# Performance work log

Hardware: AMD Instinct MI355X
Metric: run time of the kernel (lower is better)

## Reference

```python
import jax, jax.numpy as jnp
import numpy as np

NF = 64   # num_feat
DG = 8    # deformable_groups (also conv groups)
B, H, W = 4, 96, 96
K = 9     # 3x3 kernel positions


def _conv(x, w, b, padding=1, dilation=1, groups=1):
    out = jax.lax.conv_general_dilated(
        x, w, (1, 1), [(padding, padding), (padding, padding)],
        rhs_dilation=(dilation, dilation),
        dimension_numbers=('NCHW', 'OIHW', 'NCHW'),
        feature_group_count=groups)
    return out + b[None, :, None, None]


def _lrelu(t):
    return jnp.where(t >= 0, t, 0.1 * t)


def _cat_align(a, b):
    # channel-interleaved concat: [a0,b0,a1,b1,...]
    Bn, k, h, w = a.shape
    return jnp.stack([a, b], axis=2).reshape(Bn, 2 * k, h, w)


def _deform_conv(x, offset, mask, weight, bias, dilation, padding):
    # DCNv2 modulated deformable conv, stride 1.
    Bn, C, h, w = x.shape
    Cpg = C // DG
    off = offset.reshape(Bn, DG, K, 2, h, w)          # (dy, dx) per group/kernel pos
    m = mask.reshape(Bn, DG, K, h, w)
    ky = (jnp.repeat(jnp.arange(3), 3) * dilation - padding).astype(x.dtype)  # (K,)
    kx = (jnp.tile(jnp.arange(3), 3) * dilation - padding).astype(x.dtype)
    hs = jnp.arange(h, dtype=x.dtype)
    ws = jnp.arange(w, dtype=x.dtype)
    py = off[:, :, :, 0] + ky[None, None, :, None, None] + hs[None, None, None, :, None]
    px = off[:, :, :, 1] + kx[None, None, :, None, None] + ws[None, None, None, None, :]
    y0f = jnp.floor(py); x0f = jnp.floor(px)
    ly = (py - y0f)[:, :, None]  # broadcast over Cpg
    lx = (px - x0f)[:, :, None]
    y0 = y0f.astype(jnp.int32); x0 = x0f.astype(jnp.int32)
    xg = x.reshape(Bn, DG, Cpg, h * w)

    def gather(yi, xi):
        inb = ((yi >= 0) & (yi < h) & (xi >= 0) & (xi < w))
        idx = (jnp.clip(yi, 0, h - 1) * w + jnp.clip(xi, 0, w - 1)).reshape(Bn, DG, 1, K * h * w)
        v = jnp.take_along_axis(xg, jnp.broadcast_to(idx, (Bn, DG, Cpg, K * h * w)), axis=3)
        return v.reshape(Bn, DG, Cpg, K, h, w) * inb[:, :, None].astype(x.dtype)

    v00 = gather(y0, x0); v01 = gather(y0, x0 + 1)
    v10 = gather(y0 + 1, x0); v11 = gather(y0 + 1, x0 + 1)
    val = (v00 * (1 - ly) * (1 - lx) + v01 * (1 - ly) * lx
           + v10 * ly * (1 - lx) + v11 * ly * lx) * m[:, :, None]
    sampled = val.reshape(Bn, C, K, h, w)
    out = jnp.einsum('bckhw,ock->bohw', sampled, weight.reshape(weight.shape[0], C, K))
    return out + bias[None, :, None, None]


def _dcn(x, off_feat, om_w, om_b, w, b, dilation):
    pad = dilation  # int(3/2)*dilation
    out = _conv(off_feat, om_w, om_b, padding=pad, dilation=dilation)
    o1, o2, msk = jnp.split(out, 3, axis=1)
    offset = jnp.concatenate([o1, o2], axis=1)
    mask = jax.nn.sigmoid(msk)
    return _deform_conv(x, offset, mask, w, b, dilation, pad)


def setup_inputs() -> dict:
    key = jax.random.key(0)
    ks = iter(jax.random.split(key, 64))
    def rn(shape, s=0.05):
        return jax.random.normal(next(ks), shape, jnp.float32) * s
    d = {}
    d['nbr_feat'] = jax.random.normal(next(ks), (B, NF, H, W), jnp.float32)
    d['ref_feat'] = jax.random.normal(next(ks), (B, NF, H, W), jnp.float32)
    for lv, has3 in [('l3', False), ('l2', True), ('l1', True)]:
        d[f'oc1_w_{lv}'] = rn((NF, 2 * NF // DG, 3, 3)); d[f'oc1_b_{lv}'] = rn((NF,))
        oc2_in = 2 * NF if has3 else NF
        d[f'oc2_w_{lv}'] = rn((NF, oc2_in // DG, 3, 3)); d[f'oc2_b_{lv}'] = rn((NF,))
        if has3:
            d[f'oc3_w_{lv}'] = rn((NF, NF // DG, 3, 3)); d[f'oc3_b_{lv}'] = rn((NF,))
            d[f'fc_w_{lv}'] = rn((NF, 2 * NF // DG, 3, 3)); d[f'fc_b_{lv}'] = rn((NF,))
        d[f'om_w_{lv}'] = rn((DG * 3 * K, NF, 3, 3), 0.01); d[f'om_b_{lv}'] = rn((DG * 3 * K,), 0.01)
        d[f'dcn_w_{lv}'] = rn((NF, NF, 3, 3)); d[f'dcn_b_{lv}'] = rn((NF,))
    d['cas_oc1_w'] = rn((NF, 2 * NF // DG, 3, 3)); d['cas_oc1_b'] = rn((NF,))
    d['cas_oc2_w'] = rn((NF, NF // DG, 3, 3)); d['cas_oc2_b'] = rn((NF,))
    d['cas_om_w'] = rn((DG * 3 * K, NF, 3, 3), 0.01); d['cas_om_b'] = rn((DG * 3 * K,), 0.01)
    d['cas_w'] = rn((NF, NF, 3, 3)); d['cas_b'] = rn((NF,))
    return d


def reference(nbr_feat, ref_feat,
              oc1_w_l3, oc1_b_l3, oc2_w_l3, oc2_b_l3, om_w_l3, om_b_l3, dcn_w_l3, dcn_b_l3,
              oc1_w_l2, oc1_b_l2, oc2_w_l2, oc2_b_l2, oc3_w_l2, oc3_b_l2, fc_w_l2, fc_b_l2,
              om_w_l2, om_b_l2, dcn_w_l2, dcn_b_l2,
              oc1_w_l1, oc1_b_l1, oc2_w_l1, oc2_b_l1, oc3_w_l1, oc3_b_l1, fc_w_l1, fc_b_l1,
              om_w_l1, om_b_l1, dcn_w_l1, dcn_b_l1,
              cas_oc1_w, cas_oc1_b, cas_oc2_w, cas_oc2_b, cas_om_w, cas_om_b, cas_w, cas_b):
    # level 3 (dilation 5)
    off = _lrelu(_conv(_cat_align(nbr_feat, ref_feat), oc1_w_l3, oc1_b_l3, groups=DG))
    off = _lrelu(_conv(off, oc2_w_l3, oc2_b_l3, groups=DG))
    feat = _lrelu(_dcn(nbr_feat, off, om_w_l3, om_b_l3, dcn_w_l3, dcn_b_l3, 5))
    to, tf = off, feat
    # level 2 (dilation 3)
    off = _lrelu(_conv(_cat_align(nbr_feat, ref_feat), oc1_w_l2, oc1_b_l2, groups=DG))
    off = _lrelu(_conv(_cat_align(off, to), oc2_w_l2, oc2_b_l2, groups=DG))
    off = _lrelu(_conv(off, oc3_w_l2, oc3_b_l2, groups=DG))
    feat = _dcn(nbr_feat, off, om_w_l2, om_b_l2, dcn_w_l2, dcn_b_l2, 3)
    feat = _lrelu(_conv(_cat_align(feat, tf), fc_w_l2, fc_b_l2, groups=DG))
    to, tf = off, feat
    # level 1 (dilation 1), no lrelu on feat
    off = _lrelu(_conv(_cat_align(nbr_feat, ref_feat), oc1_w_l1, oc1_b_l1, groups=DG))
    off = _lrelu(_conv(_cat_align(off, to), oc2_w_l1, oc2_b_l1, groups=DG))
    off = _lrelu(_conv(off, oc3_w_l1, oc3_b_l1, groups=DG))
    feat = _dcn(nbr_feat, off, om_w_l1, om_b_l1, dcn_w_l1, dcn_b_l1, 1)
    feat = _conv(_cat_align(feat, tf), fc_w_l1, fc_b_l1, groups=DG)
    # cascade
    off = _cat_align(feat, ref_feat)
    off = _lrelu(_conv(_lrelu(_conv(off, cas_oc1_w, cas_oc1_b, groups=DG)), cas_oc2_w, cas_oc2_b, groups=DG))
    feat = _lrelu(_dcn(feat, off, cas_om_w, cas_om_b, cas_w, cas_b, 1))
    return feat
```

## Files before the change

### kernel.cpp

```cpp
#include <hip/hip_runtime.h>

#define BATCH 4
#define NFEAT 64
#define DGRP 8
#define HH 96
#define WW 96
#define HWP (HH*WW)

typedef short short4a __attribute__((ext_vector_type(4)));
typedef short short8 __attribute__((ext_vector_type(8)));
typedef float f32x4 __attribute__((ext_vector_type(4)));
typedef float f32x16 __attribute__((ext_vector_type(16)));

__device__ inline short f2bf(float f) {
  union { float f; unsigned u; } v; v.f = f;
  unsigned r = v.u + 0x7fff + ((v.u >> 16) & 1);
  return (short)(r >> 16);
}
__device__ inline float bf2f(short s) {
  return __uint_as_float(((unsigned)(unsigned short)s) << 16);
}

__global__ __launch_bounds__(256) void prep_om(
    const float* __restrict__ s0, const float* __restrict__ s1,
    const float* __restrict__ s2, const float* __restrict__ s3,
    short* __restrict__ dst) {
  int gid = blockIdx.x * 256 + threadIdx.x;
  if (gid >= 4 * 147456) return;
  int t = gid / 147456, r = gid % 147456;
  int tile = r / 18432, r2 = r % 18432;
  int kk = r2 / 512, r3 = r2 % 512;
  int lane = r3 / 8, j = r3 % 8;
  int col = lane & 31, half = lane >> 5;
  int oc = tile * 32 + col;
  int k = kk * 16 + half * 8 + j;
  int p = k >> 6, c = k & 63;
  const float* s = (t == 0) ? s0 : (t == 1) ? s1 : (t == 2) ? s2 : s3;
  float v = (oc < 216) ? s[(size_t)oc * 576 + c * 9 + p] : 0.f;
  dst[gid] = f2bf(v);
}

__global__ __launch_bounds__(256) void prep_dcnw(
    const float* __restrict__ s0, const float* __restrict__ s1,
    const float* __restrict__ s2, const float* __restrict__ s3,
    short* __restrict__ dst) {
  int gid = blockIdx.x * 256 + threadIdx.x;
  if (gid >= 4 * 36864) return;
  int t = gid / 36864, r = gid % 36864;
  int tile = r / 18432, r2 = r % 18432;
  int kk = r2 / 512, r3 = r2 % 512;
  int lane = r3 / 8, j = r3 % 8;
  int col = lane & 31, half = lane >> 5;
  int oc = tile * 32 + col;
  int k = kk * 16 + half * 8 + j;
  int p = k >> 6, c = k & 63;
  const float* s = (t == 0) ? s0 : (t == 1) ? s1 : (t == 2) ? s2 : s3;
  dst[gid] = f2bf(s[(size_t)oc * 576 + c * 9 + p]);
}

struct GwArgs {
  const float* src[12];
  int cat[12];
  int base[13];
};

__global__ __launch_bounds__(256) void prep_gw(GwArgs a, short* __restrict__ dst) {
  int gid = blockIdx.x * 256 + threadIdx.x;
  if (gid >= a.base[12]) return;
  int t = 0;
  while (gid >= a.base[t + 1]) ++t;
  int r = gid - a.base[t];
  const float* s = a.src[t];
  const int tsz = a.cat[t] ? 4608 : 2560;
  int tile = r / tsz, r2 = r % tsz;
  int kk = r2 / 512, r3 = r2 % 512;
  int lane = r3 >> 3, j = r3 & 7;
  int m = lane & 15, quad = lane >> 4;
  int oc = tile * 16 + m;
  int j32 = quad * 8 + j;
  float val = 0.f;
  if (a.cat[t]) {
    int gsel = j32 >> 4, ssel = (j32 >> 3) & 1, ch8 = j32 & 7;
    if (gsel == (m >> 3)) val = s[oc * 144 + (2 * ch8 + ssel) * 9 + kk];
  } else {
    int tapsel = j32 >> 4, gsel = (j32 >> 3) & 1, ch8 = j32 & 7;
    int p = 2 * kk + tapsel;
    if (p < 9 && gsel == (m >> 3)) val = s[oc * 72 + ch8 * 9 + p];
  }
  dst[gid] = f2bf(val);
}

__global__ __launch_bounds__(256) void transpose_bf16(
    const float* __restrict__ in0, short* __restrict__ out0,
    const float* __restrict__ in1, short* __restrict__ out1) {
  const float* in = blockIdx.z ? in1 : in0;
  short* out = blockIdx.z ? out1 : out0;
  __shared__ float s[64][65];
  const int p0 = blockIdx.x * 64;
  const int b = blockIdx.y;
  const int tx = threadIdx.x, ty = threadIdx.y;
  for (int c = ty; c < 64; c += 4)
    s[c][tx] = in[((size_t)b * NFEAT + c) * HWP + p0 + tx];
  __syncthreads();
  for (int p = ty; p < 64; p += 4)
    out[((size_t)b * HWP + p0 + p) * NFEAT + tx] = f2bf(s[tx][p]);
}

template <bool CAT, bool LRELU>
__device__ __forceinline__ void gconv_body(
    const short* __restrict__ in0, const short* __restrict__ in1,
    const short* __restrict__ Wsh, const float* __restrict__ bias,
    short* __restrict__ out, int pixbase, int b) {
  const int lane = threadIdx.x, t = threadIdx.y;
  const int n = lane & 15, quad = lane >> 4;
  constexpr int NKK = CAT ? 9 : 5;

  short8 A[NKK];
#pragma unroll
  for (int kk = 0; kk < NKK; ++kk)
    A[kk] = *(const short8*)(Wsh + ((size_t)(t * NKK + kk) * 64 + lane) * 8);

  const short* sb;
  if (CAT) {
    sb = ((quad & 1) ? in1 : in0) + (size_t)b * HWP * 64 + (2 * t + (quad >> 1)) * 8;
  } else {
    sb = in0 + (size_t)b * HWP * 64 + (2 * t + (quad & 1)) * 8;
  }

  f32x4 acc[2] = {};
#pragma unroll
  for (int nt = 0; nt < 2; ++nt) {
    const int pix = pixbase + nt * 16 + n;
    const int yp = pix / WW, xp = pix % WW;
#pragma unroll
    for (int kk = 0; kk < NKK; ++kk) {
      const int p = CAT ? kk : (2 * kk + (quad >> 1));
      short8 B = {0, 0, 0, 0, 0, 0, 0, 0};
      if (p < 9) {
        const int sy = yp + p / 3 - 1, sx = xp + p % 3 - 1;
        if (((unsigned)sy < (unsigned)HH) && ((unsigned)sx < (unsigned)WW))
          B = *(const short8*)(sb + (size_t)(sy * WW + sx) * 64);
      }
      acc[nt] = __builtin_amdgcn_mfma_f32_16x16x32_bf16(A[kk], B, acc[nt], 0, 0, 0);
    }
  }

  const int ocb = t * 16 + quad * 4;
  const float b0 = bias[ocb], b1 = bias[ocb + 1], b2 = bias[ocb + 2], b3 = bias[ocb + 3];
#pragma unroll
  for (int nt = 0; nt < 2; ++nt) {
    float v0 = acc[nt][0] + b0, v1 = acc[nt][1] + b1;
    float v2 = acc[nt][2] + b2, v3 = acc[nt][3] + b3;
    if (LRELU) {
      v0 = (v0 >= 0.f) ? v0 : 0.1f * v0;
      v1 = (v1 >= 0.f) ? v1 : 0.1f * v1;
      v2 = (v2 >= 0.f) ? v2 : 0.1f * v2;
      v3 = (v3 >= 0.f) ? v3 : 0.1f * v3;
    }
    short4a pk = {f2bf(v0), f2bf(v1), f2bf(v2), f2bf(v3)};
    *(short4a*)(out + ((size_t)b * HWP + pixbase + nt * 16 + n) * 64 + ocb) = pk;
  }
}

template <bool CAT, bool LRELU>
__global__ __launch_bounds__(256) void gconv_mfma(
    const short* __restrict__ in0, const short* __restrict__ in1,
    const short* __restrict__ Wsh, const float* __restrict__ bias,
    short* __restrict__ out) {
  gconv_body<CAT, LRELU>(in0, in1, Wsh, bias, out, blockIdx.x * 32, blockIdx.y);
}

struct Oc1Args {
  const short* W[3];
  const float* bias[3];
  short* out[3];
};

__global__ __launch_bounds__(256) void gconv_oc1x3(
    const short* __restrict__ in0, const short* __restrict__ in1, Oc1Args a) {
  const int job = blockIdx.z;
  gconv_body<true, true>(in0, in1, a.W[job], a.bias[job], a.out[job],
                         blockIdx.x * 32, blockIdx.y);
}

template <int D, bool LRELU, bool PMOUT>
__global__ __launch_bounds__(256) void omdcn_fused(
    const short* __restrict__ omIn,
    const short* __restrict__ xT,
    const short* __restrict__ Wom,
    const float* __restrict__ obias,
    const short* __restrict__ Wd,
    const float* __restrict__ bias,
    void* __restrict__ outv) {
  __shared__ __align__(16) char smem[18432 + 13824];
  short* Ls = (short*)smem;
  short* om_lds = (short*)(smem + 18432);
  float* red = (float*)(smem + 18432);

  const int tx = threadIdx.x, ty = threadIdx.y;
  const int lid = ty * 32 + tx;
  const int lane = lid & 63, w = lid >> 6;
  const int col = lane & 31, half = lane >> 5;
  const int pb = blockIdx.x, b = blockIdx.y;
  const int pixbase = pb * 32;

  {
    const short* pixb = omIn + (size_t)b * HWP * 64;
    const short* aP0 = Wom + ((size_t)(w * 36) * 64 + lane) * 8;
    const short* aP1 = Wom + ((size_t)((w + 4) * 36) * 64 + lane) * 8;
    const int pix = pixbase + col;
    const int yp = pix / WW, xp = pix % WW;
    f32x16 acc0 = {}, acc1 = {};
#pragma unroll
    for (int p = 0; p < 9; ++p) {
      const int sy = yp + (p / 3 - 1) * D, sx = xp + (p % 3 - 1) * D;
      const bool valid = ((unsigned)sy < (unsigned)HH) && ((unsigned)sx < (unsigned)WW);
      const short* bsrc = pixb + (size_t)(sy * WW + sx) * 64 + half * 8;
#pragma unroll
      for (int q = 0; q < 4; ++q) {
        const int kk = p * 4 + q;
        short8 B = {0, 0, 0, 0, 0, 0, 0, 0};
        if (valid) B = *(const short8*)(bsrc + q * 16);
        short8 A0 = *(const short8*)(aP0 + (size_t)kk * 512);
        short8 A1 = *(const short8*)(aP1 + (size_t)kk * 512);
        acc0 = __builtin_amdgcn_mfma_f32_32x32x16_bf16(A0, B, acc0, 0, 0, 0);
        acc1 = __builtin_amdgcn_mfma_f32_32x32x16_bf16(A1, B, acc1, 0, 0, 0);
      }
    }
#pragma unroll
    for (int r = 0; r < 16; ++r) {
      const int rrow = (r & 3) + 8 * (r >> 2) + 4 * half;
      const int oc0 = w * 32 + rrow;
      om_lds[oc0 * 32 + col] = f2bf(acc0[r] + obias[oc0]);
      const int oc1 = (w + 4) * 32 + rrow;
      if (oc1 < 216)
        om_lds[oc1 * 32 + col] = f2bf(acc1[r] + obias[oc1]);
    }
  }
  __syncthreads();

  const int dg = ty;
  const int pixS = pixbase + tx;
  const int ypS = pixS / WW, xpS = pixS % WW;
  const short* xb = xT + (size_t)b * HWP * 64 + dg * 8;
  short* Sp = Ls + (size_t)((dg & 1) * 32 + tx) * 8;

  auto sample_k = [&](int k, int slotbase) {
    float dy = bf2f(om_lds[(dg * 18 + 2 * k) * 32 + tx]);
    float dxv = bf2f(om_lds[(dg * 18 + 2 * k + 1) * 32 + tx]);
    float mr = bf2f(om_lds[(144 + dg * 9 + k) * 32 + tx]);
    float m = 1.f / (1.f + __expf(-mr));
    float py = (float)(ypS + (k / 3 - 1) * D) + dy;
    float px_ = (float)(xpS + (k % 3 - 1) * D) + dxv;
    float y0f = floorf(py), x0f = floorf(px_);
    float ly = py - y0f, lx = px_ - x0f;
    int y0 = (int)y0f, x0 = (int)x0f;
    int y1 = y0 + 1, x1 = x0 + 1;
    bool vy0 = (unsigned)y0 < (unsigned)HH, vy1 = (unsigned)y1 < (unsigned)HH;
    bool vx0 = (unsigned)x0 < (unsigned)WW, vx1 = (unsigned)x1 < (unsigned)WW;
    int cy0 = min(max(y0, 0), HH - 1), cy1 = min(max(y1, 0), HH - 1);
    int cx0 = min(max(x0, 0), WW - 1), cx1 = min(max(x1, 0), WW - 1);
    float w00 = (vy0 && vx0) ? (1.f - ly) * (1.f - lx) * m : 0.f;
    float w01 = (vy0 && vx1) ? (1.f - ly) * lx * m : 0.f;
    float w10 = (vy1 && vx0) ? ly * (1.f - lx) * m : 0.f;
    float w11 = (vy1 && vx1) ? ly * lx * m : 0.f;
    short8 s00 = *(const short8*)(xb + (size_t)(cy0 * WW + cx0) * 64);
    short8 s01 = *(const short8*)(xb + (size_t)(cy0 * WW + cx1) * 64);
    short8 s10 = *(const short8*)(xb + (size_t)(cy1 * WW + cx0) * 64);
    short8 s11 = *(const short8*)(xb + (size_t)(cy1 * WW + cx1) * 64);
    short8 pk;
#pragma unroll
    for (int cl = 0; cl < 8; ++cl) {
      float v = w00 * bf2f(s00[cl]) + w01 * bf2f(s01[cl]) +
                w10 * bf2f(s10[cl]) + w11 * bf2f(s11[cl]);
      pk[cl] = f2bf(v);
    }
    const int slot = k * 4 + (dg >> 1) - slotbase;
    *(short8*)(Sp + (size_t)slot * 512) = pk;
  };

  const int octile = w & 1, kh = w >> 1;
  const short* aPd = Wd + ((size_t)(octile * 36) * 64 + lane) * 8;
  const short* bPd = Ls + (size_t)lane * 8;
  f32x16 accd = {};

#pragma unroll
  for (int k = 0; k < 4; ++k) sample_k(k, 0);
  if (dg < 4) sample_k(4, 0);
  __syncthreads();
#pragma unroll
  for (int i = 0; i < 9; ++i) {
    const int kkg = kh * 9 + i;
    short8 A = *(const short8*)(aPd + (size_t)kkg * 512);
    short8 B = *(const short8*)(bPd + (size_t)kkg * 512);
    accd = __builtin_amdgcn_mfma_f32_32x32x16_bf16(A, B, accd, 0, 0, 0);
  }
  __syncthreads();

  if (dg >= 4) sample_k(4, 18);
#pragma unroll
  for (int k = 5; k < 9; ++k) sample_k(k, 18);
  __syncthreads();
#pragma unroll
  for (int i = 0; i < 9; ++i) {
    const int kkg = 18 + kh * 9 + i;
    const int kkl = kh * 9 + i;
    short8 A = *(const short8*)(aPd + (size_t)kkg * 512);
    short8 B = *(const short8*)(bPd + (size_t)kkl * 512);
    accd = __builtin_amdgcn_mfma_f32_32x32x16_bf16(A, B, accd, 0, 0, 0);
  }

  const int pix = pixbase + col;
  if (kh == 1) {
#pragma unroll
    for (int r = 0; r < 16; ++r) red[(octile * 64 + lane) * 17 + r] = accd[r];
  }
  __syncthreads();
  if (kh == 0) {
    if (PMOUT) {
      short* out = (short*)outv;
#pragma unroll
      for (int rg = 0; rg < 4; ++rg) {
        short4a pk;
#pragma unroll
        for (int i = 0; i < 4; ++i) {
          const int r = rg * 4 + i;
          const int oc = octile * 32 + i + 8 * rg + 4 * half;
          float v = accd[r] + red[(octile * 64 + lane) * 17 + r] + bias[oc];
          if (LRELU) v = (v >= 0.f) ? v : 0.1f * v;
          pk[i] = f2bf(v);
        }
        *(short4a*)(out + ((size_t)b * HWP + pix) * 64 + octile * 32 + 8 * rg + 4 * half) = pk;
      }
    } else {
      float* out = (float*)outv;
#pragma unroll
      for (int r = 0; r < 16; ++r) {
        const int oc = octile * 32 + (r & 3) + 8 * (r >> 2) + 4 * half;
        float v = accd[r] + red[(octile * 64 + lane) * 17 + r] + bias[oc];
        if (LRELU) v = (v >= 0.f) ? v : 0.1f * v;
        out[((size_t)b * NFEAT + oc) * HWP + pix] = v;
      }
    }
  }
}

extern "C" void kernel_launch(void* const* d_in, const int* in_sizes, int n_in,
                              void* d_out, int out_size, void* d_ws, size_t ws_size,
                              hipStream_t stream) {
  const float* nbr = (const float*)d_in[0];
  const float* ref = (const float*)d_in[1];
  auto f = [&](int i) { return (const float*)d_in[i]; };

  short* s0 = (short*)d_ws;
  const size_t PM = (size_t)BATCH * HWP * 64;
  short* omB = s0;
  short* refT = omB + 7962624;
  short* pmA = refT + PM;
  short* pmB = pmA + PM;
  short* pmC = pmB + PM;
  short* pmD = pmC + PM;
  short* pmE = pmD + PM;
  short* pmF = pmE + PM;
  short* pmG = pmF + PM;
  short* wbf = pmG + PM;
  short* wdcn = wbf + 589824;
  short* wgc = wdcn + 147456;
  short* nbrT = (short*)d_out;

  prep_om<<<(4 * 147456 + 255) / 256, 256, 0, stream>>>(f(6), f(18), f(30), f(38), wbf);
  prep_dcnw<<<(4 * 36864 + 255) / 256, 256, 0, stream>>>(f(8), f(20), f(32), f(40), wdcn);

  static const int gSrc[12] = {2, 4, 10, 12, 14, 16, 22, 24, 26, 28, 34, 36};
  static const int gCat[12] = {1, 0, 1, 1, 0, 1, 1, 1, 0, 1, 1, 0};
  GwArgs ga;
  int gb = 0;
  const short* wg[12];
  for (int t = 0; t < 12; ++t) {
    ga.src[t] = f(gSrc[t]);
    ga.cat[t] = gCat[t];
    ga.base[t] = gb;
    wg[t] = wgc + gb;
    gb += gCat[t] ? 18432 : 10240;
  }
  ga.base[12] = gb;
  prep_gw<<<(gb + 255) / 256, 256, 0, stream>>>(ga, wgc);

  short* wbf_l3 = wbf;
  short* wbf_l2 = wbf + 147456;
  short* wbf_l1 = wbf + 2 * 147456;
  short* wbf_cas = wbf + 3 * 147456;
  short* wd_l3 = wdcn;
  short* wd_l2 = wdcn + 36864;
  short* wd_l1 = wdcn + 2 * 36864;
  short* wd_cas = wdcn + 3 * 36864;

  dim3 gcGrid(288, BATCH), gcBlk(64, 4);
  dim3 oc1Grid(288, BATCH, 3);
  dim3 fGrid(288, BATCH), fBlk(32, 8);
  dim3 trGrid(HWP / 64, BATCH, 2), trBlk(64, 4);

  transpose_bf16<<<trGrid, trBlk, 0, stream>>>(nbr, nbrT, ref, refT);

  Oc1Args oa;
  oa.W[0] = wg[0]; oa.bias[0] = f(3);  oa.out[0] = pmA;
  oa.W[1] = wg[2]; oa.bias[1] = f(11); oa.out[1] = pmF;
  oa.W[2] = wg[6]; oa.bias[2] = f(23); oa.out[2] = pmG;
  gconv_oc1x3<<<oc1Grid, gcBlk, 0, stream>>>(nbrT, refT, oa);

  gconv_mfma<false, true><<<gcGrid, gcBlk, 0, stream>>>(pmA, nullptr, wg[1], f(5), pmB);
  omdcn_fused<5, true, true><<<fGrid, fBlk, 0, stream>>>(
      pmB, nbrT, wbf_l3, f(7), wd_l3, f(9), pmC);

  gconv_mfma<true, true><<<gcGrid, gcBlk, 0, stream>>>(pmF, pmB, wg[3], f(13), pmD);
  gconv_mfma<false, true><<<gcGrid, gcBlk, 0, stream>>>(pmD, nullptr, wg[4], f(15), pmE);
  omdcn_fused<3, false, true><<<fGrid, fBlk, 0, stream>>>(
      pmE, nbrT, wbf_l2, f(19), wd_l2, f(21), pmD);
  gconv_mfma<true, true><<<gcGrid, gcBlk, 0, stream>>>(pmD, pmC, wg[5], f(17), pmA);

  gconv_mfma<true, true><<<gcGrid, gcBlk, 0, stream>>>(pmG, pmE, wg[7], f(25), pmB);
  gconv_mfma<false, true><<<gcGrid, gcBlk, 0, stream>>>(pmB, nullptr, wg[8], f(27), pmC);
  omdcn_fused<1, false, true><<<fGrid, fBlk, 0, stream>>>(
      pmC, nbrT, wbf_l1, f(31), wd_l1, f(33), pmD);
  gconv_mfma<true, false><<<gcGrid, gcBlk, 0, stream>>>(pmD, pmA, wg[9], f(29), pmB);

  gconv_mfma<true, true><<<gcGrid, gcBlk, 0, stream>>>(pmB, refT, wg[10], f(35), pmC);
  gconv_mfma<false, true><<<gcGrid, gcBlk, 0, stream>>>(pmC, nullptr, wg[11], f(37), pmD);
  omdcn_fused<1, true, false><<<fGrid, fBlk, 0, stream>>>(
      pmD, pmB, wbf_cas, f(39), wd_cas, f(41), (float*)d_out);
}
```

Baseline: 581.2 us.

## Double fused offset-mask/DCN block to 512 threads, single-pass sampling with 4-way K split

The fused offset-mask conv plus deformable conv kernel now uses 16 warps-of-32 rows (8 wave64s) per block instead of 8. Each wave computes one 32-channel tile of the offset/mask conv instead of two. The bilinear sampling of all 9 kernel positions now happens in one pass into a doubled LDS buffer, split across two thread halves, which removes the second sample-then-MFMA phase and its barriers. The DCN GEMM K dimension is split four ways with a 3-way LDS reduction. This raises parallelism and latency hiding per block, at the cost of more LDS per block (about 50KB), which may reduce blocks per CU.

After: 651.9 us. 12.2% more time.

```diff
diff --git a/kernel.cpp b/kernel.cpp
--- a/kernel.cpp
+++ b/kernel.cpp
@@ -184,7 +184,7 @@
 }
 
 template <int D, bool LRELU, bool PMOUT>
-__global__ __launch_bounds__(256) void omdcn_fused(
+__global__ __launch_bounds__(512) void omdcn_fused(
     const short* __restrict__ omIn,
     const short* __restrict__ xT,
     const short* __restrict__ Wom,
@@ -192,10 +192,10 @@
     const short* __restrict__ Wd,
     const float* __restrict__ bias,
     void* __restrict__ outv) {
-  __shared__ __align__(16) char smem[18432 + 13824];
+  __shared__ __align__(16) char smem[36864 + 13824];
   short* Ls = (short*)smem;
-  short* om_lds = (short*)(smem + 18432);
-  float* red = (float*)(smem + 18432);
+  short* om_lds = (short*)(smem + 36864);
+  float* red = (float*)smem;
 
   const int tx = threadIdx.x, ty = threadIdx.y;
   const int lid = ty * 32 + tx;
@@ -206,11 +206,10 @@
 
   {
     const short* pixb = omIn + (size_t)b * HWP * 64;
-    const short* aP0 = Wom + ((size_t)(w * 36) * 64 + lane) * 8;
-    const short* aP1 = Wom + ((size_t)((w + 4) * 36) * 64 + lane) * 8;
+    const short* aP = Wom + ((size_t)(w * 36) * 64 + lane) * 8;
     const int pix = pixbase + col;
     const int yp = pix / WW, xp = pix % WW;
-    f32x16 acc0 = {}, acc1 = {};
+    f32x16 acc = {};
 #pragma unroll
     for (int p = 0; p < 9; ++p) {
       const int sy = yp + (p / 3 - 1) * D, sx = xp + (p % 3 - 1) * D;
@@ -221,73 +220,73 @@
         const int kk = p * 4 + q;
         short8 B = {0, 0, 0, 0, 0, 0, 0, 0};
         if (valid) B = *(const short8*)(bsrc + q * 16);
-        short8 A0 = *(const short8*)(aP0 + (size_t)kk * 512);
-        short8 A1 = *(const short8*)(aP1 + (size_t)kk * 512);
-        acc0 = __builtin_amdgcn_mfma_f32_32x32x16_bf16(A0, B, acc0, 0, 0, 0);
-        acc1 = __builtin_amdgcn_mfma_f32_32x32x16_bf16(A1, B, acc1, 0, 0, 0);
+        short8 A = *(const short8*)(aP + (size_t)kk * 512);
+        acc = __builtin_amdgcn_mfma_f32_32x32x16_bf16(A, B, acc, 0, 0, 0);
       }
     }
 #pragma unroll
     for (int r = 0; r < 16; ++r) {
       const int rrow = (r & 3) + 8 * (r >> 2) + 4 * half;
-      const int oc0 = w * 32 + rrow;
-      om_lds[oc0 * 32 + col] = f2bf(acc0[r] + obias[oc0]);
-      const int oc1 = (w + 4) * 32 + rrow;
-      if (oc1 < 216)
-        om_lds[oc1 * 32 + col] = f2bf(acc1[r] + obias[oc1]);
+      const int oc = w * 32 + rrow;
+      if (oc < 216) om_lds[oc * 32 + col] = f2bf(acc[r] + obias[oc]);
     }
   }
   __syncthreads();
 
-  const int dg = ty;
-  const int pixS = pixbase + tx;
-  const int ypS = pixS / WW, xpS = pixS % WW;
-  const short* xb = xT + (size_t)b * HWP * 64 + dg * 8;
-  short* Sp = Ls + (size_t)((dg & 1) * 32 + tx) * 8;
-
-  auto sample_k = [&](int k, int slotbase) {
-    float dy = bf2f(om_lds[(dg * 18 + 2 * k) * 32 + tx]);
-    float dxv = bf2f(om_lds[(dg * 18 + 2 * k + 1) * 32 + tx]);
-    float mr = bf2f(om_lds[(144 + dg * 9 + k) * 32 + tx]);
-    float m = 1.f / (1.f + __expf(-mr));
-    float py = (float)(ypS + (k / 3 - 1) * D) + dy;
-    float px_ = (float)(xpS + (k % 3 - 1) * D) + dxv;
-    float y0f = floorf(py), x0f = floorf(px_);
-    float ly = py - y0f, lx = px_ - x0f;
-    int y0 = (int)y0f, x0 = (int)x0f;
-    int y1 = y0 + 1, x1 = x0 + 1;
-    bool vy0 = (unsigned)y0 < (unsigned)HH, vy1 = (unsigned)y1 < (unsigned)HH;
-    bool vx0 = (unsigned)x0 < (unsigned)WW, vx1 = (unsigned)x1 < (unsigned)WW;
-    int cy0 = min(max(y0, 0), HH - 1), cy1 = min(max(y1, 0), HH - 1);
-    int cx0 = min(max(x0, 0), WW - 1), cx1 = min(max(x1, 0), WW - 1);
-    float w00 = (vy0 && vx0) ? (1.f - ly) * (1.f - lx) * m : 0.f;
-    float w01 = (vy0 && vx1) ? (1.f - ly) * lx * m : 0.f;
-    float w10 = (vy1 && vx0) ? ly * (1.f - lx) * m : 0.f;
-    float w11 = (vy1 && vx1) ? ly * lx * m : 0.f;
-    short8 s00 = *(const short8*)(xb + (size_t)(cy0 * WW + cx0) * 64);
-    short8 s01 = *(const short8*)(xb + (size_t)(cy0 * WW + cx1) * 64);
-    short8 s10 = *(const short8*)(xb + (size_t)(cy1 * WW + cx0) * 64);
-    short8 s11 = *(const short8*)(xb + (size_t)(cy1 * WW + cx1) * 64);
-    short8 pk;
-#pragma unroll
-    for (int cl = 0; cl < 8; ++cl) {
-      float v = w00 * bf2f(s00[cl]) + w01 * bf2f(s01[cl]) +
-                w10 * bf2f(s10[cl]) + w11 * bf2f(s11[cl]);
-      pk[cl] = f2bf(v);
-    }
-    const int slot = k * 4 + (dg >> 1) - slotbase;
-    *(short8*)(Sp + (size_t)slot * 512) = pk;
-  };
+  {
+    const int dg = ty & 7, th = ty >> 3;
+    const int pixS = pixbase + tx;
+    const int ypS = pixS / WW, xpS = pixS % WW;
+    const short* xb = xT + (size_t)b * HWP * 64 + dg * 8;
+    short* Sp = Ls + (size_t)((dg & 1) * 32 + tx) * 8;
+
+    auto sample_k = [&](int k) {
+      float dy = bf2f(om_lds[(dg * 18 + 2 * k) * 32 + tx]);
+      float dxv = bf2f(om_lds[(dg * 18 + 2 * k + 1) * 32 + tx]);
+      float mr = bf2f(om_lds[(144 + dg * 9 + k) * 32 + tx]);
+      float m = 1.f / (1.f + __expf(-mr));
+      float py = (float)(ypS + (k / 3 - 1) * D) + dy;
+      float px_ = (float)(xpS + (k % 3 - 1) * D) + dxv;
+      float y0f = floorf(py), x0f = floorf(px_);
+      float ly = py - y0f, lx = px_ - x0f;
+      int y0 = (int)y0f, x0 = (int)x0f;
+      int y1 = y0 + 1, x1 = x0 + 1;
+      bool vy0 = (unsigned)y0 < (unsigned)HH, vy1 = (unsigned)y1 < (unsigned)HH;
+      bool vx0 = (unsigned)x0 < (unsigned)WW, vx1 = (unsigned)x1 < (unsigned)WW;
+      int cy0 = min(max(y0, 0), HH - 1), cy1 = min(max(y1, 0), HH - 1);
+      int cx0 = min(max(x0, 0), WW - 1), cx1 = min(max(x1, 0), WW - 1);
+      float w00 = (vy0 && vx0) ? (1.f - ly) * (1.f - lx) * m : 0.f;
+      float w01 = (vy0 && vx1) ? (1.f - ly) * lx * m : 0.f;
+      float w10 = (vy1 && vx0) ? ly * (1.f - lx) * m : 0.f;
+      float w11 = (vy1 && vx1) ? ly * lx * m : 0.f;
+      short8 s00 = *(const short8*)(xb + (size_t)(cy0 * WW + cx0) * 64);
+      short8 s01 = *(const short8*)(xb + (size_t)(cy0 * WW + cx1) * 64);
+      short8 s10 = *(const short8*)(xb + (size_t)(cy1 * WW + cx0) * 64);
+      short8 s11 = *(const short8*)(xb + (size_t)(cy1 * WW + cx1) * 64);
+      short8 pk;
+#pragma unroll
+      for (int cl = 0; cl < 8; ++cl) {
+        float v = w00 * bf2f(s00[cl]) + w01 * bf2f(s01[cl]) +
+                  w10 * bf2f(s10[cl]) + w11 * bf2f(s11[cl]);
+        pk[cl] = f2bf(v);
+      }
+      const int slot = k * 4 + (dg >> 1);
+      *(short8*)(Sp + (size_t)slot * 512) = pk;
+    };
+
+    if (th == 0) {
+      sample_k(0); sample_k(1); sample_k(2); sample_k(3); sample_k(4);
+    } else {
+      sample_k(5); sample_k(6); sample_k(7); sample_k(8);
+    }
+  }
+  __syncthreads();
 
   const int octile = w & 1, kh = w >> 1;
   const short* aPd = Wd + ((size_t)(octile * 36) * 64 + lane) * 8;
   const short* bPd = Ls + (size_t)lane * 8;
+
   f32x16 accd = {};
-
-#pragma unroll
-  for (int k = 0; k < 4; ++k) sample_k(k, 0);
-  if (dg < 4) sample_k(4, 0);
-  __syncthreads();
 #pragma unroll
   for (int i = 0; i < 9; ++i) {
     const int kkg = kh * 9 + i;
@@ -297,26 +296,18 @@
   }
   __syncthreads();
 
-  if (dg >= 4) sample_k(4, 18);
-#pragma unroll
-  for (int k = 5; k < 9; ++k) sample_k(k, 18);
+  if (kh != 0) {
+    float* rp = red + (size_t)(((kh - 1) * 2 + octile) * 64 + lane) * 17;
+#pragma unroll
+    for (int r = 0; r < 16; ++r) rp[r] = accd[r];
+  }
   __syncthreads();
-#pragma unroll
-  for (int i = 0; i < 9; ++i) {
-    const int kkg = 18 + kh * 9 + i;
-    const int kkl = kh * 9 + i;
-    short8 A = *(const short8*)(aPd + (size_t)kkg * 512);
-    short8 B = *(const short8*)(bPd + (size_t)kkl * 512);
-    accd = __builtin_amdgcn_mfma_f32_32x32x16_bf16(A, B, accd, 0, 0, 0);
-  }
-
-  const int pix = pixbase + col;
-  if (kh == 1) {
-#pragma unroll
-    for (int r = 0; r < 16; ++r) red[(octile * 64 + lane) * 17 + r] = accd[r];
-  }
-  __syncthreads();
+
   if (kh == 0) {
+    const int pix = pixbase + col;
+    const float* r0 = red + (size_t)((0 * 2 + octile) * 64 + lane) * 17;
+    const float* r1 = red + (size_t)((2 + octile) * 64 + lane) * 17;
+    const float* r2 = red + (size_t)((4 + octile) * 64 + lane) * 17;
     if (PMOUT) {
       short* out = (short*)outv;
 #pragma unroll
@@ -326,7 +317,7 @@
         for (int i = 0; i < 4; ++i) {
           const int r = rg * 4 + i;
           const int oc = octile * 32 + i + 8 * rg + 4 * half;
-          float v = accd[r] + red[(octile * 64 + lane) * 17 + r] + bias[oc];
+          float v = accd[r] + r0[r] + r1[r] + r2[r] + bias[oc];
           if (LRELU) v = (v >= 0.f) ? v : 0.1f * v;
           pk[i] = f2bf(v);
         }
@@ -337,7 +328,7 @@
 #pragma unroll
       for (int r = 0; r < 16; ++r) {
         const int oc = octile * 32 + (r & 3) + 8 * (r >> 2) + 4 * half;
-        float v = accd[r] + red[(octile * 64 + lane) * 17 + r] + bias[oc];
+        float v = accd[r] + r0[r] + r1[r] + r2[r] + bias[oc];
         if (LRELU) v = (v >= 0.f) ? v : 0.1f * v;
         out[((size_t)b * NFEAT + oc) * HWP + pix] = v;
       }
@@ -397,7 +388,7 @@
 
   dim3 gcGrid(288, BATCH), gcBlk(64, 4);
   dim3 oc1Grid(288, BATCH, 3);
-  dim3 fGrid(288, BATCH), fBlk(32, 8);
+  dim3 fGrid(288, BATCH), fBlk(32, 16);
   dim3 trGrid(HWP / 64, BATCH, 2), trBlk(64, 4);
 
   transpose_bf16<<<trGrid, trBlk, 0, stream>>>(nbr, nbrT, ref, refT);
```
